# Kernel tuning notes

Measured on AMD Instinct MI355X. Metric: run time of the kernel, lower is better.

Reference implementation:

```python
import jax, jax.numpy as jnp
import numpy as np

M, N, K = 4096, 8192, 4096


def setup_inputs() -> dict:
    key = jax.random.key(0)
    k1, k2, k3, k4 = jax.random.split(key, 4)
    a = jax.random.randint(k1, (M, K), 0, 127, dtype=jnp.int32)  # int8 activations
    b = jax.random.randint(k2, (N, K), 0, 127, dtype=jnp.int32)  # int8 weights (row-major [N,K])
    alpha_row = jax.random.uniform(k3, (M, 1), dtype=jnp.float16)  # per-row dequant scale
    alpha_col = jax.random.uniform(k4, (1, N), dtype=jnp.float16)  # per-col dequant scale
    return {"a": a, "b": b, "alpha_row": alpha_row, "alpha_col": alpha_col}


def reference(a, b, alpha_row, alpha_col):
    # x = a @ b.T in fp32 (int8 values upcast), then rescale by outer product of scales
    x = jnp.matmul(a.astype(jnp.float32), b.astype(jnp.float32).T)  # [M, N]
    scale = alpha_row.astype(jnp.float32) * alpha_col.astype(jnp.float32)  # [M, N] via broadcast
    out = x * scale
    return out.astype(jnp.float16)
```

## Files before the change

kernel.cpp:

```cpp
#include <hip/hip_runtime.h>
#include <cstdint>
#include <cstddef>

#define M_DIM 4096
#define N_DIM 8192
#define K_DIM 4096

typedef __attribute__((ext_vector_type(4))) int int4v;

__global__ void __launch_bounds__(256) pack_frag(const int* __restrict__ a,
                                                 const int* __restrict__ b,
                                                 unsigned char* __restrict__ pa,
                                                 unsigned char* __restrict__ pb) {
    size_t t = (size_t)blockIdx.x * 256 + threadIdx.x;
    const size_t NA = (size_t)(M_DIM / 16) * (K_DIM / 64) * 64;
    const int* __restrict__ src;
    unsigned char* __restrict__ dst;
    if (t < NA) {
        src = a; dst = pa;
    } else {
        src = b; dst = pb; t -= NA;
    }
    const int l = (int)(t & 63);
    const int s = (int)((t >> 6) & 63);
    const int p = (int)(t >> 12);
    const int* g = src + ((size_t)(16 * p + (l & 15))) * K_DIM + s * 64 + (l >> 4) * 16;
    const int4v* g4 = (const int4v*)g;
    int4v o;
#pragma unroll
    for (int q = 0; q < 4; ++q) {
        int4v v = g4[q];
        o[q] = (v[0] & 0xff) | ((v[1] & 0xff) << 8) | ((v[2] & 0xff) << 16) | (v[3] << 24);
    }
    ((int4v*)dst)[t] = o;
}

__device__ inline void async_copy16(const unsigned char* g, unsigned char* l) {
    __builtin_amdgcn_global_load_lds(
        (const __attribute__((address_space(1))) void*)g,
        (__attribute__((address_space(3))) void*)l,
        16, 0, 0);
}

__global__ void __launch_bounds__(512, 2) gemm_i8(const unsigned char* __restrict__ Ap,
                                                  const unsigned char* __restrict__ Bp,
                                                  const _Float16* __restrict__ arow,
                                                  const _Float16* __restrict__ acol,
                                                  _Float16* __restrict__ Cout) {
    __shared__ __align__(16) unsigned char As[4 * 16384];
    __shared__ __align__(16) unsigned char Bs[4 * 16384];

    const int tid  = threadIdx.x;
    const int lane = tid & 63;
    const int wave = tid >> 6;
    const int bn   = blockIdx.x;
    const int bm   = blockIdx.y;

    const int pm0 = (wave & 3) * 4;
    const int pn0 = (wave >> 2) * 8;

    const unsigned char* ag[2];
    const unsigned char* bg[2];
    int slo[2];
#pragma unroll
    for (int r = 0; r < 2; ++r) {
        const int p = 2 * wave + r;
        ag[r]  = Ap + (size_t)(bm * 16 + p) * 65536 + lane * 16;
        bg[r]  = Bp + (size_t)(bn * 16 + p) * 65536 + lane * 16;
        slo[r] = p * 1024;
    }

    const int a_off = pm0 * 1024 + lane * 16;
    const int b_off = pn0 * 1024 + lane * 16;

    int4v acc[4][8];
#pragma unroll
    for (int i = 0; i < 4; ++i)
#pragma unroll
        for (int j = 0; j < 8; ++j) acc[i][j] = (int4v)0;

    const int NT = K_DIM / 64;

#pragma unroll
    for (int r = 0; r < 2; ++r) {
        async_copy16(ag[r], As + slo[r]);
        async_copy16(bg[r], Bs + slo[r]);
        async_copy16(ag[r] + 1024, As + 16384 + slo[r]);
        async_copy16(bg[r] + 1024, Bs + 16384 + slo[r]);
    }
    __syncthreads();

    for (int T = 0; T < NT; T += 2) {
        if (T + 2 < NT) {
            const size_t gko = (size_t)(T + 2) * 1024;
            const int buf = ((T + 2) & 3) * 16384;
#pragma unroll
            for (int r = 0; r < 2; ++r) {
                async_copy16(ag[r] + gko, As + buf + slo[r]);
                async_copy16(bg[r] + gko, Bs + buf + slo[r]);
            }
            const size_t gko3 = gko + 1024;
            const int buf3 = ((T + 3) & 3) * 16384;
#pragma unroll
            for (int r = 0; r < 2; ++r) {
                async_copy16(ag[r] + gko3, As + buf3 + slo[r]);
                async_copy16(bg[r] + gko3, Bs + buf3 + slo[r]);
            }
        }

#pragma unroll
        for (int u = 0; u < 2; ++u) {
            const int cur = ((T + u) & 3) * 16384;
            const unsigned char* Ac = As + cur;
            const unsigned char* Bc = Bs + cur;

            int4v af[4], bf[8];
#pragma unroll
            for (int i = 0; i < 4; ++i)
                af[i] = *(const int4v*)(Ac + a_off + i * 1024);
#pragma unroll
            for (int j = 0; j < 8; ++j)
                bf[j] = *(const int4v*)(Bc + b_off + j * 1024);

#pragma unroll
            for (int i = 0; i < 4; ++i)
#pragma unroll
                for (int j = 0; j < 8; ++j)
                    acc[i][j] = __builtin_amdgcn_mfma_i32_16x16x64_i8(af[i], bf[j],
                                                                      acc[i][j], 0, 0, 0);
        }

        __syncthreads();
    }

    const int gcol0 = bn * 256 + pn0 * 16 + (lane & 15);
    float ac8[8];
#pragma unroll
    for (int j = 0; j < 8; ++j) ac8[j] = (float)acol[gcol0 + j * 16];

    const size_t grow0 = (size_t)bm * 256 + pm0 * 16 + (lane >> 4) * 4;
#pragma unroll
    for (int i = 0; i < 4; ++i) {
#pragma unroll
        for (int r = 0; r < 4; ++r) {
            const size_t row = grow0 + i * 16 + r;
            const float ar = (float)arow[row];
            _Float16* outp = Cout + row * (size_t)N_DIM + gcol0;
#pragma unroll
            for (int j = 0; j < 8; ++j) {
                float v = (float)acc[i][j][r] * ar * ac8[j];
                outp[j * 16] = (_Float16)v;
            }
        }
    }
}

extern "C" void kernel_launch(void* const* d_in, const int* in_sizes, int n_in,
                              void* d_out, int out_size, void* d_ws, size_t ws_size,
                              hipStream_t stream) {
    const int* a = (const int*)d_in[0];
    const int* b = (const int*)d_in[1];
    const _Float16* ar = (const _Float16*)d_in[2];
    const _Float16* ac = (const _Float16*)d_in[3];
    _Float16* out = (_Float16*)d_out;

    unsigned char* pa = (unsigned char*)d_ws;
    unsigned char* pb = pa + (size_t)M_DIM * K_DIM;

    const size_t total_frag = (size_t)(M_DIM / 16 + N_DIM / 16) * (K_DIM / 64) * 64;
    pack_frag<<<(int)(total_frag / 256), 256, 0, stream>>>(a, b, pa, pb);

    dim3 grid(N_DIM / 256, M_DIM / 256);
    gemm_i8<<<grid, 512, 0, stream>>>(pa, pb, ar, ac, out);
}
```

Measured before the change: 374.0 us.

## Switch int8 GEMM to 32x32x32 MFMA with matching fragment packing

Replaces the 16x16x64 int8 MFMA with the 32x32x32 variant. The pack kernel now emits 32-row fragments, and the LDS tiling, per-wave fragment loads and epilogue row/column mapping are reworked to fit. Each wave now covers a 64x128 tile with 2x4 accumulators of 16 ints. The larger instruction needs fewer fragment LDS reads per unit of MMA work, which cuts LDS bandwidth pressure. In exchange the per-instruction latency is longer and the epilogue store pattern changes.

```diff
diff --git a/kernel.cpp b/kernel.cpp
--- a/kernel.cpp
+++ b/kernel.cpp
@@ -7,13 +7,14 @@
 #define K_DIM 4096
 
 typedef __attribute__((ext_vector_type(4))) int int4v;
+typedef __attribute__((ext_vector_type(16))) int int16v;
 
 __global__ void __launch_bounds__(256) pack_frag(const int* __restrict__ a,
                                                  const int* __restrict__ b,
                                                  unsigned char* __restrict__ pa,
                                                  unsigned char* __restrict__ pb) {
     size_t t = (size_t)blockIdx.x * 256 + threadIdx.x;
-    const size_t NA = (size_t)(M_DIM / 16) * (K_DIM / 64) * 64;
+    const size_t NA = (size_t)(M_DIM / 32) * (K_DIM / 32) * 64;
     const int* __restrict__ src;
     unsigned char* __restrict__ dst;
     if (t < NA) {
@@ -22,9 +23,9 @@
         src = b; dst = pb; t -= NA;
     }
     const int l = (int)(t & 63);
-    const int s = (int)((t >> 6) & 63);
-    const int p = (int)(t >> 12);
-    const int* g = src + ((size_t)(16 * p + (l & 15))) * K_DIM + s * 64 + (l >> 4) * 16;
+    const int s = (int)((t >> 6) & (K_DIM / 32 - 1));
+    const int p = (int)(t >> 13);
+    const int* g = src + ((size_t)(32 * p + (l & 31))) * K_DIM + s * 32 + (l >> 5) * 16;
     const int4v* g4 = (const int4v*)g;
     int4v o;
 #pragma unroll
@@ -56,100 +57,94 @@
     const int bn   = blockIdx.x;
     const int bm   = blockIdx.y;
 
-    const int pm0 = (wave & 3) * 4;
-    const int pn0 = (wave >> 2) * 8;
+    const int pm0 = (wave & 3) * 2;
+    const int pn0 = (wave >> 2) * 4;
 
-    const unsigned char* ag[2];
-    const unsigned char* bg[2];
-    int slo[2];
+    const unsigned char* ag = Ap + (size_t)(bm * 8 + wave) * 131072 + lane * 16;
+    const unsigned char* bg = Bp + (size_t)(bn * 8 + wave) * 131072 + lane * 16;
+    const int slo = wave * 2048;
+
+    const int a_off = pm0 * 2048 + lane * 16;
+    const int b_off = pn0 * 2048 + lane * 16;
+
+    int16v acc[2][4];
 #pragma unroll
-    for (int r = 0; r < 2; ++r) {
-        const int p = 2 * wave + r;
-        ag[r]  = Ap + (size_t)(bm * 16 + p) * 65536 + lane * 16;
-        bg[r]  = Bp + (size_t)(bn * 16 + p) * 65536 + lane * 16;
-        slo[r] = p * 1024;
-    }
-
-    const int a_off = pm0 * 1024 + lane * 16;
-    const int b_off = pn0 * 1024 + lane * 16;
-
-    int4v acc[4][8];
+    for (int i = 0; i < 2; ++i)
 #pragma unroll
-    for (int i = 0; i < 4; ++i)
-#pragma unroll
-        for (int j = 0; j < 8; ++j) acc[i][j] = (int4v)0;
+        for (int j = 0; j < 4; ++j) acc[i][j] = (int16v)0;
 
     const int NT = K_DIM / 64;
 
 #pragma unroll
-    for (int r = 0; r < 2; ++r) {
-        async_copy16(ag[r], As + slo[r]);
-        async_copy16(bg[r], Bs + slo[r]);
-        async_copy16(ag[r] + 1024, As + 16384 + slo[r]);
-        async_copy16(bg[r] + 1024, Bs + 16384 + slo[r]);
+    for (int u = 0; u < 2; ++u) {
+        async_copy16(ag + u * 1024,        As + slo + u * 1024);
+        async_copy16(bg + u * 1024,        Bs + slo + u * 1024);
+        async_copy16(ag + 2048 + u * 1024, As + 16384 + slo + u * 1024);
+        async_copy16(bg + 2048 + u * 1024, Bs + 16384 + slo + u * 1024);
     }
     __syncthreads();
 
     for (int T = 0; T < NT; T += 2) {
         if (T + 2 < NT) {
-            const size_t gko = (size_t)(T + 2) * 1024;
-            const int buf = ((T + 2) & 3) * 16384;
 #pragma unroll
-            for (int r = 0; r < 2; ++r) {
-                async_copy16(ag[r] + gko, As + buf + slo[r]);
-                async_copy16(bg[r] + gko, Bs + buf + slo[r]);
-            }
-            const size_t gko3 = gko + 1024;
-            const int buf3 = ((T + 3) & 3) * 16384;
+            for (int w = 2; w < 4; ++w) {
+                const size_t gko = (size_t)(T + w) * 2048;
+                const int buf = ((T + w) & 3) * 16384;
 #pragma unroll
-            for (int r = 0; r < 2; ++r) {
-                async_copy16(ag[r] + gko3, As + buf3 + slo[r]);
-                async_copy16(bg[r] + gko3, Bs + buf3 + slo[r]);
+                for (int u = 0; u < 2; ++u) {
+                    async_copy16(ag + gko + u * 1024, As + buf + slo + u * 1024);
+                    async_copy16(bg + gko + u * 1024, Bs + buf + slo + u * 1024);
+                }
             }
         }
 
 #pragma unroll
-        for (int u = 0; u < 2; ++u) {
-            const int cur = ((T + u) & 3) * 16384;
+        for (int v = 0; v < 2; ++v) {
+            const int cur = ((T + v) & 3) * 16384;
             const unsigned char* Ac = As + cur;
             const unsigned char* Bc = Bs + cur;
 
-            int4v af[4], bf[8];
+            int4v af[2][2], bf[2][4];
 #pragma unroll
-            for (int i = 0; i < 4; ++i)
-                af[i] = *(const int4v*)(Ac + a_off + i * 1024);
+            for (int u = 0; u < 2; ++u) {
 #pragma unroll
-            for (int j = 0; j < 8; ++j)
-                bf[j] = *(const int4v*)(Bc + b_off + j * 1024);
+                for (int i = 0; i < 2; ++i)
+                    af[u][i] = *(const int4v*)(Ac + a_off + i * 2048 + u * 1024);
+#pragma unroll
+                for (int j = 0; j < 4; ++j)
+                    bf[u][j] = *(const int4v*)(Bc + b_off + j * 2048 + u * 1024);
+            }
 
 #pragma unroll
-            for (int i = 0; i < 4; ++i)
+            for (int u = 0; u < 2; ++u)
 #pragma unroll
-                for (int j = 0; j < 8; ++j)
-                    acc[i][j] = __builtin_amdgcn_mfma_i32_16x16x64_i8(af[i], bf[j],
-                                                                      acc[i][j], 0, 0, 0);
+                for (int i = 0; i < 2; ++i)
+#pragma unroll
+                    for (int j = 0; j < 4; ++j)
+                        acc[i][j] = __builtin_amdgcn_mfma_i32_32x32x32_i8(
+                            af[u][i], bf[u][j], acc[i][j], 0, 0, 0);
         }
 
         __syncthreads();
     }
 
-    const int gcol0 = bn * 256 + pn0 * 16 + (lane & 15);
-    float ac8[8];
+    const int gcol0 = bn * 256 + pn0 * 32 + (lane & 31);
+    float ac4[4];
 #pragma unroll
-    for (int j = 0; j < 8; ++j) ac8[j] = (float)acol[gcol0 + j * 16];
+    for (int j = 0; j < 4; ++j) ac4[j] = (float)acol[gcol0 + j * 32];
 
-    const size_t grow0 = (size_t)bm * 256 + pm0 * 16 + (lane >> 4) * 4;
+    const size_t rbase = (size_t)bm * 256 + pm0 * 32 + 4 * (lane >> 5);
 #pragma unroll
-    for (int i = 0; i < 4; ++i) {
+    for (int i = 0; i < 2; ++i) {
 #pragma unroll
-        for (int r = 0; r < 4; ++r) {
-            const size_t row = grow0 + i * 16 + r;
+        for (int r = 0; r < 16; ++r) {
+            const size_t row = rbase + i * 32 + (r & 3) + 8 * (r >> 2);
             const float ar = (float)arow[row];
             _Float16* outp = Cout + row * (size_t)N_DIM + gcol0;
 #pragma unroll
-            for (int j = 0; j < 8; ++j) {
-                float v = (float)acc[i][j][r] * ar * ac8[j];
-                outp[j * 16] = (_Float16)v;
+            for (int j = 0; j < 4; ++j) {
+                float v = (float)acc[i][j][r] * ar * ac4[j];
+                outp[j * 32] = (_Float16)v;
             }
         }
     }
@@ -167,7 +162,7 @@
     unsigned char* pa = (unsigned char*)d_ws;
     unsigned char* pb = pa + (size_t)M_DIM * K_DIM;
 
-    const size_t total_frag = (size_t)(M_DIM / 16 + N_DIM / 16) * (K_DIM / 64) * 64;
+    const size_t total_frag = (size_t)(M_DIM / 32 + N_DIM / 32) * (K_DIM / 32) * 64;
     pack_frag<<<(int)(total_frag / 256), 256, 0, stream>>>(a, b, pa, pb);
 
     dim3 grid(N_DIM / 256, M_DIM / 256);
```

New measurement: 381.7 us. +2.1%, slower.
